# Performance work log

Hardware: AMD Instinct MI355X
Metric: run time of the kernel (lower is better)

## Reference

```python
import jax, jax.numpy as jnp
import numpy as np

H = 64          # HIDDEN_SIZE
D = 300         # WORD_VEC_DIMS
L = 3           # NUM_LSTM_LAYERS
B = 256
T = 512


def _uniform(key, shape, scale):
    return jax.random.uniform(key, shape, jnp.float32, -scale, scale)


def setup_inputs() -> dict:
    key = jax.random.key(0)
    keys = jax.random.split(key, 32)
    s = 1.0 / np.sqrt(H)  # torch LSTM/Linear init scale
    inp = {
        "input": jax.random.normal(keys[0], (B, T, D), jnp.float32),
        "h_0": jnp.zeros((L, B, H), jnp.float32),
        "c_0": jnp.zeros((L, B, H), jnp.float32),
    }
    k = 1
    for l in range(L):
        din = D if l == 0 else H
        inp[f"wih{l}"] = _uniform(keys[k], (4 * H, din), s); k += 1
        inp[f"whh{l}"] = _uniform(keys[k], (4 * H, H), s); k += 1
        inp[f"bih{l}"] = _uniform(keys[k], (4 * H,), s); k += 1
        inp[f"bhh{l}"] = _uniform(keys[k], (4 * H,), s); k += 1
    inp["w1"] = _uniform(keys[k], (H, H), s); k += 1
    inp["b1"] = _uniform(keys[k], (H,), s); k += 1
    inp["w2"] = _uniform(keys[k], (D, H), s); k += 1
    inp["b2"] = _uniform(keys[k], (D,), s); k += 1
    return inp


def _lstm_layer(x_tbd, h0, c0, Wih, Whh, bih, bhh):
    # x_tbd: [T, B, Din]; precompute input projection outside the scan
    xp = jnp.einsum('tbd,gd->tbg', x_tbd, Wih) + bih  # [T, B, 4H]

    def step(carry, xt):
        h, c = carry
        g = xt + h @ Whh.T + bhh
        i, f, gg, o = jnp.split(g, 4, axis=-1)  # torch gate order: i,f,g,o
        c = jax.nn.sigmoid(f) * c + jax.nn.sigmoid(i) * jnp.tanh(gg)
        h = jax.nn.sigmoid(o) * jnp.tanh(c)
        return (h, c), h

    (hT, cT), hs = jax.lax.scan(step, (h0, c0), xp)
    return hs, hT, cT  # hs: [T, B, H]


def reference(input, h_0, c_0, wih0, whh0, bih0, bhh0, wih1, whh1, bih1, bhh1,
              wih2, whh2, bih2, bhh2, w1, b1, w2, b2):
    wih = [wih0, wih1, wih2]
    whh = [whh0, whh1, whh2]
    bih = [bih0, bih1, bih2]
    bhh = [bhh0, bhh1, bhh2]
    x = jnp.transpose(input, (1, 0, 2))  # [T, B, D]
    hs_n, cs_n = [], []
    for l in range(L):
        x, hT, cT = _lstm_layer(x, h_0[l], c_0[l], wih[l], whh[l], bih[l], bhh[l])
        hs_n.append(hT)
        cs_n.append(cT)
    # x is now [T, B, H] == output.permute(1, 0, 2) of the batch_first LSTM.
    # Faithfully replicate the original permute+view reordering:
    flat = x.reshape(-1, H)                       # time-major flatten
    y = jnp.tanh(flat @ w1.T + b1) @ w2.T + b2    # MLP head
    out = y.reshape(input.shape[0], -1, D)        # reinterpreted batch-major
    h_n = jnp.stack(hs_n)
    c_n = jnp.stack(cs_n)
    return out, h_n, c_n
```

## Files before the change

kernel.cpp:

```cpp
#include <hip/hip_runtime.h>
#include <math.h>


#define TT 512
#define BB 256
#define DD 300
#define HH 64
#define MM (TT * BB)
#define XP 256
#define TC 128
#define NC (TT / TC)

__device__ __forceinline__ float bf2f(unsigned short u) {
    return __uint_as_float(((unsigned int)u) << 16);
}
__device__ __forceinline__ unsigned short f2bf(float f) {
    unsigned int x = __float_as_uint(f);
    x += 0x7FFFu + ((x >> 16) & 1u);
    return (unsigned short)(x >> 16);
}
__device__ __forceinline__ float sigm(float x) { return 1.f / (1.f + __expf(-x)); }
__device__ __forceinline__ float tanh_f(float x) { return 1.f - 2.f / (__expf(2.f * x) + 1.f); }

__device__ __forceinline__ float ld1(const void* p, long long i, int md) {
    return md ? ((const float*)p)[i] : bf2f(((const unsigned short*)p)[i]);
}
__device__ __forceinline__ void ld4v(float* d, const void* p, long long i, int md) {
    if (md) {
        float4 v = *(const float4*)((const float*)p + i);
        d[0] = v.x; d[1] = v.y; d[2] = v.z; d[3] = v.w;
    } else {
        ushort4 u = *(const ushort4*)((const unsigned short*)p + i);
        d[0] = bf2f(u.x); d[1] = bf2f(u.y); d[2] = bf2f(u.z); d[3] = bf2f(u.w);
    }
}

#define FMA4x4(a, bv)                                        \
    acc[0][0] = fmaf((a).x, (bv).x, acc[0][0]);              \
    acc[0][1] = fmaf((a).x, (bv).y, acc[0][1]);              \
    acc[0][2] = fmaf((a).x, (bv).z, acc[0][2]);              \
    acc[0][3] = fmaf((a).x, (bv).w, acc[0][3]);              \
    acc[1][0] = fmaf((a).y, (bv).x, acc[1][0]);              \
    acc[1][1] = fmaf((a).y, (bv).y, acc[1][1]);              \
    acc[1][2] = fmaf((a).y, (bv).z, acc[1][2]);              \
    acc[1][3] = fmaf((a).y, (bv).w, acc[1][3]);              \
    acc[2][0] = fmaf((a).z, (bv).x, acc[2][0]);              \
    acc[2][1] = fmaf((a).z, (bv).y, acc[2][1]);              \
    acc[2][2] = fmaf((a).z, (bv).z, acc[2][2]);              \
    acc[2][3] = fmaf((a).z, (bv).w, acc[2][3]);              \
    acc[3][0] = fmaf((a).w, (bv).x, acc[3][0]);              \
    acc[3][1] = fmaf((a).w, (bv).y, acc[3][1]);              \
    acc[3][2] = fmaf((a).w, (bv).z, acc[3][2]);              \
    acc[3][3] = fmaf((a).w, (bv).w, acc[3][3]);

__global__ void detect_kernel(const void* inp, int* mode) {
    if (threadIdx.x == 0 && blockIdx.x == 0) {
        const unsigned short* u = (const unsigned short*)inp;
        int bad = 0;
        for (int i = 0; i < 256; ++i) {
            float f = bf2f(u[i]);
            if (!(f == f) || fabsf(f) > 1e6f) ++bad;
        }
        *mode = (bad >= 4) ? 1 : 0;
    }
}

__global__ __launch_bounds__(256) void init_state(
    const void* h0, const void* c0, float* hstate, float* cstate, const int* modep)
{
    const int md = *modep;
    int i = blockIdx.x * 256 + threadIdx.x;
    if (i < 3 * BB * HH) {
        hstate[i] = ld1(h0, i, md);
        cstate[i] = ld1(c0, i, md);
    }
}

__global__ __launch_bounds__(256) void final_state(
    const float* hstate, const float* cstate, void* out, const int* modep)
{
    const int md = *modep;
    int i = blockIdx.x * 256 + threadIdx.x;
    const long long base = (long long)MM * DD;
    if (i < 3 * BB * HH) {
        if (md) {
            ((float*)out)[base + i] = hstate[i];
            ((float*)out)[base + 3 * BB * HH + i] = cstate[i];
        } else {
            ((unsigned short*)out)[base + i] = f2bf(hstate[i]);
            ((unsigned short*)out)[base + 3 * BB * HH + i] = f2bf(cstate[i]);
        }
    }
}

__global__ __launch_bounds__(256) void proj0_chunk(
    const void* __restrict__ inp, const void* __restrict__ wih,
    const void* __restrict__ bih, const void* __restrict__ bhh,
    float* __restrict__ xp, const int* modep, int chunk)
{
    const int md = *modep;
    __shared__ __align__(16) float At[64][68];
    __shared__ __align__(16) float Wt[64][68];
    const int tid = threadIdx.x;
    const int lr = tid >> 2;
    const int lc = (tid & 3) * 16;
    const int tx = tid & 15, ty = tid >> 4;
    const int m0 = blockIdx.x * 64, n0 = blockIdx.y * 64;
    const int ml = m0 + lr;
    const int b = ml & 255;
    const int t = chunk * TC + (ml >> 8);
    const long long abase = (long long)b * (TT * DD) + (long long)t * DD;
    const long long wbase = (long long)(n0 + lr) * DD;
    float acc[4][4] = {{0.f,0.f,0.f,0.f},{0.f,0.f,0.f,0.f},{0.f,0.f,0.f,0.f},{0.f,0.f,0.f,0.f}};
    for (int k0 = 0; k0 < DD; k0 += 64) {
        if (k0 + lc + 15 < DD) {
            #pragma unroll
            for (int q = 0; q < 4; ++q) {
                float va[4], vw[4];
                ld4v(va, inp, abase + k0 + lc + q * 4, md);
                ld4v(vw, wih, wbase + k0 + lc + q * 4, md);
                #pragma unroll
                for (int e = 0; e < 4; ++e) {
                    At[lc + q * 4 + e][lr] = va[e];
                    Wt[lc + q * 4 + e][lr] = vw[e];
                }
            }
        } else {
            #pragma unroll
            for (int q = 0; q < 16; ++q) {
                int k = k0 + lc + q;
                At[lc + q][lr] = (k < DD) ? ld1(inp, abase + k, md) : 0.f;
                Wt[lc + q][lr] = (k < DD) ? ld1(wih, wbase + k, md) : 0.f;
            }
        }
        __syncthreads();
        #pragma unroll 16
        for (int k = 0; k < 64; ++k) {
            float4 a = *(const float4*)&At[k][ty * 4];
            float4 bv = *(const float4*)&Wt[k][tx * 4];
            FMA4x4(a, bv)
        }
        __syncthreads();
    }
    float bias[4];
    #pragma unroll
    for (int j = 0; j < 4; ++j) {
        int n = n0 + tx * 4 + j;
        bias[j] = ld1(bih, n, md) + ld1(bhh, n, md);
    }
    #pragma unroll
    for (int i = 0; i < 4; ++i) {
        long long row = m0 + ty * 4 + i;
        float4 o = make_float4(acc[i][0] + bias[0], acc[i][1] + bias[1],
                               acc[i][2] + bias[2], acc[i][3] + bias[3]);
        *(float4*)(xp + row * XP + n0 + tx * 4) = o;
    }
}

__global__ __launch_bounds__(256) void projh_chunk(
    const float* __restrict__ A, const void* __restrict__ wih,
    const void* __restrict__ bih, const void* __restrict__ bhh,
    float* __restrict__ xp, const int* modep)
{
    const int md = *modep;
    __shared__ __align__(16) float At[64][68];
    __shared__ __align__(16) float Wt[64][68];
    const int tid = threadIdx.x;
    const int lr = tid >> 2;
    const int lc = (tid & 3) * 16;
    const int tx = tid & 15, ty = tid >> 4;
    const int m0 = blockIdx.x * 64, n0 = blockIdx.y * 64;
    float acc[4][4] = {{0.f,0.f,0.f,0.f},{0.f,0.f,0.f,0.f},{0.f,0.f,0.f,0.f},{0.f,0.f,0.f,0.f}};
    #pragma unroll
    for (int q = 0; q < 4; ++q) {
        float4 av = *(const float4*)(A + (long long)(m0 + lr) * HH + lc + q * 4);
        float vw[4];
        ld4v(vw, wih, (long long)(n0 + lr) * HH + lc + q * 4, md);
        At[lc+q*4+0][lr]=av.x; At[lc+q*4+1][lr]=av.y; At[lc+q*4+2][lr]=av.z; At[lc+q*4+3][lr]=av.w;
        Wt[lc+q*4+0][lr]=vw[0]; Wt[lc+q*4+1][lr]=vw[1]; Wt[lc+q*4+2][lr]=vw[2]; Wt[lc+q*4+3][lr]=vw[3];
    }
    __syncthreads();
    #pragma unroll 16
    for (int k = 0; k < 64; ++k) {
        float4 a = *(const float4*)&At[k][ty * 4];
        float4 bv = *(const float4*)&Wt[k][tx * 4];
        FMA4x4(a, bv)
    }
    float bias[4];
    #pragma unroll
    for (int j = 0; j < 4; ++j) {
        int n = n0 + tx * 4 + j;
        bias[j] = ld1(bih, n, md) + ld1(bhh, n, md);
    }
    #pragma unroll
    for (int i = 0; i < 4; ++i) {
        long long row = m0 + ty * 4 + i;
        float4 o = make_float4(acc[i][0] + bias[0], acc[i][1] + bias[1],
                               acc[i][2] + bias[2], acc[i][3] + bias[3]);
        *(float4*)(xp + row * XP + n0 + tx * 4) = o;
    }
}

__global__ __launch_bounds__(256) void scan_chunk(
    const float* __restrict__ xp, float* __restrict__ hs,
    const void* __restrict__ whh,
    float* __restrict__ hstate, float* __restrict__ cstate, const int* modep)
{
    const int md = *modep;
    const int b = blockIdx.x;
    const int j = threadIdx.x;
    const int g = ((j & 3) << 6) | (j >> 2);
    const int m = j & 63;
    __shared__ __align__(16) float h_s[64];
    __shared__ __align__(16) float g_s[2][256];
    float w[64];
    #pragma unroll
    for (int q = 0; q < 16; ++q) {
        float v[4];
        ld4v(v, whh, (long long)g * HH + q * 4, md);
        w[4*q+0]=v[0]; w[4*q+1]=v[1]; w[4*q+2]=v[2]; w[4*q+3]=v[3];
    }
    float c = cstate[b * HH + m];
    h_s[m] = hstate[b * HH + m];
    float hval = h_s[m];

    const int type = j & 3;
    const float aa = (type == 2) ? 2.f : 1.f;
    const float cc = 1.f - aa;

    const long long xbase = (long long)b * XP + g;
    const long long xstep = (long long)BB * XP;
    float xc[8], xn[8];
    #pragma unroll
    for (int p = 0; p < 8; ++p) xc[p] = xp[xbase + (long long)p * xstep];

    for (int tg = 0; tg < TC; tg += 8) {
        if (tg + 8 < TC) {
            #pragma unroll
            for (int p = 0; p < 8; ++p)
                xn[p] = xp[xbase + (long long)(tg + 8 + p) * xstep];
        }
        #pragma unroll
        for (int u = 0; u < 8; ++u) {
            const int t = tg + u;
            float a0 = xc[u], a1 = 0.f, a2 = 0.f, a3 = 0.f;
            const float4* h4 = (const float4*)h_s;
            #pragma unroll
            for (int q = 0; q < 16; ++q) {
                float4 hv = h4[q];
                a0 = fmaf(hv.x, w[4*q+0], a0);
                a1 = fmaf(hv.y, w[4*q+1], a1);
                a2 = fmaf(hv.z, w[4*q+2], a2);
                a3 = fmaf(hv.w, w[4*q+3], a3);
            }
            float gr = (a0 + a1) + (a2 + a3);
            float s = 1.f / (1.f + __expf(-aa * gr));
            g_s[t & 1][j] = fmaf(aa, s, cc);
            asm volatile("s_waitcnt lgkmcnt(0)\n\ts_barrier" ::: "memory");
            float4 gv = *(const float4*)&g_s[t & 1][4 * m];
            c = gv.y * c + gv.x * gv.z;
            hval = gv.w * tanh_f(c);
            h_s[m] = hval;
            if (j < 64) hs[((long long)t * BB + b) * HH + m] = hval;
        }
        #pragma unroll
        for (int p = 0; p < 8; ++p) xc[p] = xn[p];
    }
    if (j < 64) {
        hstate[b * HH + m] = hval;
        cstate[b * HH + m] = c;
    }
}

__global__ __launch_bounds__(256) void head_chunk(
    const float* __restrict__ hs, const void* __restrict__ w1,
    const void* __restrict__ b1, const void* __restrict__ w2,
    const void* __restrict__ b2, void* __restrict__ out,
    const int* modep, int chunk)
{
    const int md = *modep;
    __shared__ __align__(16) float Ht[64][68];
    __shared__ __align__(16) float Wt[64][68];
    __shared__ __align__(16) float Zt[64][68];
    const int tid = threadIdx.x;
    const int lr = tid >> 2;
    const int lc = (tid & 3) * 16;
    const int tx = tid & 15, ty = tid >> 4;
    const int m0 = blockIdx.x * 64;
    const long long gbase = (long long)chunk * TC * BB;
    #pragma unroll
    for (int q = 0; q < 4; ++q) {
        float4 av = *(const float4*)(hs + (long long)(m0 + lr) * HH + lc + q * 4);
        float vw[4];
        ld4v(vw, w1, (long long)lr * HH + lc + q * 4, md);
        Ht[lc+q*4+0][lr]=av.x; Ht[lc+q*4+1][lr]=av.y; Ht[lc+q*4+2][lr]=av.z; Ht[lc+q*4+3][lr]=av.w;
        Wt[lc+q*4+0][lr]=vw[0]; Wt[lc+q*4+1][lr]=vw[1]; Wt[lc+q*4+2][lr]=vw[2]; Wt[lc+q*4+3][lr]=vw[3];
    }
    __syncthreads();
    {
        float acc[4][4] = {{0.f,0.f,0.f,0.f},{0.f,0.f,0.f,0.f},{0.f,0.f,0.f,0.f},{0.f,0.f,0.f,0.f}};
        #pragma unroll 16
        for (int k = 0; k < 64; ++k) {
            float4 a = *(const float4*)&Ht[k][ty * 4];
            float4 bv = *(const float4*)&Wt[k][tx * 4];
            FMA4x4(a, bv)
        }
        #pragma unroll
        for (int jj = 0; jj < 4; ++jj) {
            float bb = ld1(b1, tx * 4 + jj, md);
            #pragma unroll
            for (int ii = 0; ii < 4; ++ii)
                Zt[tx * 4 + jj][ty * 4 + ii] = tanh_f(acc[ii][jj] + bb);
        }
    }
    __syncthreads();
    for (int dt = 0; dt < 5; ++dt) {
        const int d0 = dt * 64;
        if (d0 + lr < DD) {
            #pragma unroll
            for (int q = 0; q < 4; ++q) {
                float vw[4];
                ld4v(vw, w2, (long long)(d0 + lr) * HH + lc + q * 4, md);
                Wt[lc+q*4+0][lr]=vw[0]; Wt[lc+q*4+1][lr]=vw[1];
                Wt[lc+q*4+2][lr]=vw[2]; Wt[lc+q*4+3][lr]=vw[3];
            }
        }
        __syncthreads();
        float acc[4][4] = {{0.f,0.f,0.f,0.f},{0.f,0.f,0.f,0.f},{0.f,0.f,0.f,0.f},{0.f,0.f,0.f,0.f}};
        #pragma unroll 16
        for (int k = 0; k < 64; ++k) {
            float4 a = *(const float4*)&Zt[k][ty * 4];
            float4 bv = *(const float4*)&Wt[k][tx * 4];
            FMA4x4(a, bv)
        }
        const int d = d0 + tx * 4;
        if (d < DD) {
            float bb0 = ld1(b2, d + 0, md), bb1 = ld1(b2, d + 1, md);
            float bb2v = ld1(b2, d + 2, md), bb3 = ld1(b2, d + 3, md);
            #pragma unroll
            for (int ii = 0; ii < 4; ++ii) {
                long long row = gbase + m0 + ty * 4 + ii;
                float o0 = acc[ii][0] + bb0, o1 = acc[ii][1] + bb1;
                float o2 = acc[ii][2] + bb2v, o3 = acc[ii][3] + bb3;
                if (md) {
                    *(float4*)((float*)out + row * DD + d) = make_float4(o0, o1, o2, o3);
                } else {
                    ushort4 o;
                    o.x = f2bf(o0); o.y = f2bf(o1); o.z = f2bf(o2); o.w = f2bf(o3);
                    *(ushort4*)((unsigned short*)out + row * DD + d) = o;
                }
            }
        }
        __syncthreads();
    }
}

extern "C" void kernel_launch(void* const* d_in, const int* in_sizes, int n_in,
                              void* d_out, int out_size, void* d_ws, size_t ws_size,
                              hipStream_t stream)
{
    const void* inp  = d_in[0];
    const void* h0   = d_in[1];
    const void* c0   = d_in[2];
    const void* wih0 = d_in[3];
    const void* whh0 = d_in[4];
    const void* bih0 = d_in[5];
    const void* bhh0 = d_in[6];
    const void* wih1 = d_in[7];
    const void* whh1 = d_in[8];
    const void* bih1 = d_in[9];
    const void* bhh1 = d_in[10];
    const void* wih2 = d_in[11];
    const void* whh2 = d_in[12];
    const void* bih2 = d_in[13];
    const void* bhh2 = d_in[14];
    const void* w1   = d_in[15];
    const void* b1   = d_in[16];
    const void* w2   = d_in[17];
    const void* b2   = d_in[18];

    int* mode = (int*)d_ws;
    float* wsf = (float*)d_ws;
    float* hstate = wsf + 16;
    float* cstate = hstate + 3 * BB * HH;
    float* xp  = cstate + 3 * BB * HH;
    float* hs0 = xp + (size_t)TC * BB * XP;
    float* hs1 = hs0 + (size_t)TC * BB * HH;
    float* hs2 = hs1 + (size_t)TC * BB * HH;

    detect_kernel<<<1, 64, 0, stream>>>(inp, mode);
    init_state<<<192, 256, 0, stream>>>(h0, c0, hstate, cstate, mode);

    for (int c = 0; c < NC; ++c) {
        proj0_chunk<<<dim3(TC * BB / 64, 4), 256, 0, stream>>>(
            inp, wih0, bih0, bhh0, xp, mode, c);
        scan_chunk<<<BB, 256, 0, stream>>>(
            xp, hs0, whh0, hstate, cstate, mode);
        projh_chunk<<<dim3(TC * BB / 64, 4), 256, 0, stream>>>(
            hs0, wih1, bih1, bhh1, xp, mode);
        scan_chunk<<<BB, 256, 0, stream>>>(
            xp, hs1, whh1, hstate + BB * HH, cstate + BB * HH, mode);
        projh_chunk<<<dim3(TC * BB / 64, 4), 256, 0, stream>>>(
            hs1, wih2, bih2, bhh2, xp, mode);
        scan_chunk<<<BB, 256, 0, stream>>>(
            xp, hs2, whh2, hstate + 2 * BB * HH, cstate + 2 * BB * HH, mode);
        head_chunk<<<TC * BB / 64, 256, 0, stream>>>(
            hs2, w1, b1, w2, b2, d_out, mode, c);
    }
    final_state<<<192, 256, 0, stream>>>(hstate, cstate, d_out, mode);
}
```

Measured before the change: 1.974 ms.

## Use bf16 MFMA for input projections and MLP head in bf16 mode

```diff
diff --git a/kernel.cpp b/kernel.cpp
--- a/kernel.cpp
+++ b/kernel.cpp
@@ -11,6 +11,9 @@
 #define TC 128
 #define NC (TT / TC)
 
+typedef __attribute__((ext_vector_type(8))) short bf16x8;
+typedef __attribute__((ext_vector_type(4))) float f32x4;
+
 __device__ __forceinline__ float bf2f(unsigned short u) {
     return __uint_as_float(((unsigned int)u) << 16);
 }
@@ -33,6 +36,10 @@
         ushort4 u = *(const ushort4*)((const unsigned short*)p + i);
         d[0] = bf2f(u.x); d[1] = bf2f(u.y); d[2] = bf2f(u.z); d[3] = bf2f(u.w);
     }
+}
+
+__device__ __forceinline__ f32x4 mfma16(bf16x8 a, bf16x8 b, f32x4 c) {
+    return __builtin_amdgcn_mfma_f32_16x16x32_bf16(a, b, c, 0, 0, 0);
 }
 
 #define FMA4x4(a, bv)                                        \
@@ -99,61 +106,134 @@
     float* __restrict__ xp, const int* modep, int chunk)
 {
     const int md = *modep;
-    __shared__ __align__(16) float At[64][68];
-    __shared__ __align__(16) float Wt[64][68];
+    __shared__ __align__(16) char smem[46080];
     const int tid = threadIdx.x;
-    const int lr = tid >> 2;
-    const int lc = (tid & 3) * 16;
-    const int tx = tid & 15, ty = tid >> 4;
-    const int m0 = blockIdx.x * 64, n0 = blockIdx.y * 64;
-    const int ml = m0 + lr;
-    const int b = ml & 255;
-    const int t = chunk * TC + (ml >> 8);
-    const long long abase = (long long)b * (TT * DD) + (long long)t * DD;
-    const long long wbase = (long long)(n0 + lr) * DD;
-    float acc[4][4] = {{0.f,0.f,0.f,0.f},{0.f,0.f,0.f,0.f},{0.f,0.f,0.f,0.f},{0.f,0.f,0.f,0.f}};
-    for (int k0 = 0; k0 < DD; k0 += 64) {
-        if (k0 + lc + 15 < DD) {
+    const int m0 = blockIdx.x * 64;
+    if (md == 0) {
+        unsigned short* As = (unsigned short*)smem;
+        unsigned short* Ws = (unsigned short*)smem + 64 * 72;
+        const int lane = tid & 63;
+        const int wv = tid >> 6;
+        const int fr = lane & 15, fq = lane >> 4;
+        const int ar = tid >> 2;
+        const int aq = (tid & 3) << 4;
+        const int ml = m0 + ar;
+        const int b = ml & 255;
+        const int t = chunk * TC + (ml >> 8);
+        const unsigned short* gA = (const unsigned short*)inp +
+            (long long)b * (TT * DD) + (long long)t * DD;
+        const unsigned short* gW = (const unsigned short*)wih + (long long)tid * DD;
+        float bias[4];
+        #pragma unroll
+        for (int nf = 0; nf < 4; ++nf) {
+            int n = wv * 64 + nf * 16 + fr;
+            bias[nf] = ld1(bih, n, 0) + ld1(bhh, n, 0);
+        }
+        f32x4 acc[4][4] = {};
+        for (int k0 = 0; k0 < 320; k0 += 64) {
             #pragma unroll
             for (int q = 0; q < 4; ++q) {
-                float va[4], vw[4];
-                ld4v(va, inp, abase + k0 + lc + q * 4, md);
-                ld4v(vw, wih, wbase + k0 + lc + q * 4, md);
-                #pragma unroll
-                for (int e = 0; e < 4; ++e) {
-                    At[lc + q * 4 + e][lr] = va[e];
-                    Wt[lc + q * 4 + e][lr] = vw[e];
-                }
-            }
-        } else {
+                int kg = k0 + aq + q * 4;
+                ushort4 v = (kg < DD) ? *(const ushort4*)(gA + kg)
+                                      : make_ushort4(0, 0, 0, 0);
+                *(ushort4*)(As + ar * 72 + aq + q * 4) = v;
+            }
             #pragma unroll
             for (int q = 0; q < 16; ++q) {
-                int k = k0 + lc + q;
-                At[lc + q][lr] = (k < DD) ? ld1(inp, abase + k, md) : 0.f;
-                Wt[lc + q][lr] = (k < DD) ? ld1(wih, wbase + k, md) : 0.f;
-            }
-        }
-        __syncthreads();
-        #pragma unroll 16
-        for (int k = 0; k < 64; ++k) {
-            float4 a = *(const float4*)&At[k][ty * 4];
-            float4 bv = *(const float4*)&Wt[k][tx * 4];
-            FMA4x4(a, bv)
-        }
-        __syncthreads();
-    }
-    float bias[4];
-    #pragma unroll
-    for (int j = 0; j < 4; ++j) {
-        int n = n0 + tx * 4 + j;
-        bias[j] = ld1(bih, n, md) + ld1(bhh, n, md);
-    }
-    #pragma unroll
-    for (int i = 0; i < 4; ++i) {
-        long long row = m0 + ty * 4 + i;
-        float4 o = make_float4(acc[i][0] + bias[0], acc[i][1] + bias[1],
-                               acc[i][2] + bias[2], acc[i][3] + bias[3]);
-        *(float4*)(xp + row * XP + n0 + tx * 4) = o;
+                int kg = k0 + q * 4;
+                ushort4 v = (kg < DD) ? *(const ushort4*)(gW + kg)
+                                      : make_ushort4(0, 0, 0, 0);
+                *(ushort4*)(Ws + tid * 72 + q * 4) = v;
+            }
+            __syncthreads();
+            #pragma unroll
+            for (int kf = 0; kf < 2; ++kf) {
+                bf16x8 bfr[4], afr[4];
+                #pragma unroll
+                for (int nf = 0; nf < 4; ++nf)
+                    bfr[nf] = *(const bf16x8*)(Ws + (wv * 64 + nf * 16 + fr) * 72 + kf * 32 + fq * 8);
+                #pragma unroll
+                for (int mf = 0; mf < 4; ++mf)
+                    afr[mf] = *(const bf16x8*)(As + (mf * 16 + fr) * 72 + kf * 32 + fq * 8);
+                #pragma unroll
+                for (int mf = 0; mf < 4; ++mf) {
+                    #pragma unroll
+                    for (int nf = 0; nf < 4; ++nf)
+                        acc[mf][nf] = mfma16(afr[mf], bfr[nf], acc[mf][nf]);
+                }
+            }
+            __syncthreads();
+        }
+        #pragma unroll
+        for (int mf = 0; mf < 4; ++mf) {
+            #pragma unroll
+            for (int nf = 0; nf < 4; ++nf) {
+                const int col = wv * 64 + nf * 16 + fr;
+                #pragma unroll
+                for (int r = 0; r < 4; ++r) {
+                    const int row = m0 + mf * 16 + fq * 4 + r;
+                    xp[(long long)row * XP + col] = acc[mf][nf][r] + bias[nf];
+                }
+            }
+        }
+    } else {
+        float (*At)[68] = (float (*)[68])smem;
+        float (*Wt)[68] = (float (*)[68])(smem + 64 * 68 * 4);
+        const int lr = tid >> 2;
+        const int lc = (tid & 3) * 16;
+        const int tx = tid & 15, ty = tid >> 4;
+        const int ml = m0 + lr;
+        const int b = ml & 255;
+        const int t = chunk * TC + (ml >> 8);
+        const long long abase = (long long)b * (TT * DD) + (long long)t * DD;
+        for (int ny = 0; ny < 4; ++ny) {
+            const int n0 = ny * 64;
+            const long long wbase = (long long)(n0 + lr) * DD;
+            float acc[4][4] = {{0.f,0.f,0.f,0.f},{0.f,0.f,0.f,0.f},{0.f,0.f,0.f,0.f},{0.f,0.f,0.f,0.f}};
+            for (int k0 = 0; k0 < DD; k0 += 64) {
+                if (k0 + lc + 15 < DD) {
+                    #pragma unroll
+                    for (int q = 0; q < 4; ++q) {
+                        float va[4], vw[4];
+                        ld4v(va, inp, abase + k0 + lc + q * 4, md);
+                        ld4v(vw, wih, wbase + k0 + lc + q * 4, md);
+                        #pragma unroll
+                        for (int e = 0; e < 4; ++e) {
+                            At[lc + q * 4 + e][lr] = va[e];
+                            Wt[lc + q * 4 + e][lr] = vw[e];
+                        }
+                    }
+                } else {
+                    #pragma unroll
+                    for (int q = 0; q < 16; ++q) {
+                        int k = k0 + lc + q;
+                        At[lc + q][lr] = (k < DD) ? ld1(inp, abase + k, md) : 0.f;
+                        Wt[lc + q][lr] = (k < DD) ? ld1(wih, wbase + k, md) : 0.f;
+                    }
+                }
+                __syncthreads();
+                #pragma unroll 16
+                for (int k = 0; k < 64; ++k) {
+                    float4 a = *(const float4*)&At[k][ty * 4];
+                    float4 bv = *(const float4*)&Wt[k][tx * 4];
+                    FMA4x4(a, bv)
+                }
+                __syncthreads();
+            }
+            float bias[4];
+            #pragma unroll
+            for (int j = 0; j < 4; ++j) {
+                int n = n0 + tx * 4 + j;
+                bias[j] = ld1(bih, n, md) + ld1(bhh, n, md);
+            }
+            #pragma unroll
+            for (int i = 0; i < 4; ++i) {
+                long long row = m0 + ty * 4 + i;
+                float4 o = make_float4(acc[i][0] + bias[0], acc[i][1] + bias[1],
+                                       acc[i][2] + bias[2], acc[i][3] + bias[3]);
+                *(float4*)(xp + row * XP + n0 + tx * 4) = o;
+            }
+        }
     }
 }
 
@@ -163,41 +243,116 @@
     float* __restrict__ xp, const int* modep)
 {
     const int md = *modep;
-    __shared__ __align__(16) float At[64][68];
-    __shared__ __align__(16) float Wt[64][68];
+    __shared__ __align__(16) char smem[55296];
     const int tid = threadIdx.x;
-    const int lr = tid >> 2;
-    const int lc = (tid & 3) * 16;
-    const int tx = tid & 15, ty = tid >> 4;
-    const int m0 = blockIdx.x * 64, n0 = blockIdx.y * 64;
-    float acc[4][4] = {{0.f,0.f,0.f,0.f},{0.f,0.f,0.f,0.f},{0.f,0.f,0.f,0.f},{0.f,0.f,0.f,0.f}};
-    #pragma unroll
-    for (int q = 0; q < 4; ++q) {
-        float4 av = *(const float4*)(A + (long long)(m0 + lr) * HH + lc + q * 4);
-        float vw[4];
-        ld4v(vw, wih, (long long)(n0 + lr) * HH + lc + q * 4, md);
-        At[lc+q*4+0][lr]=av.x; At[lc+q*4+1][lr]=av.y; At[lc+q*4+2][lr]=av.z; At[lc+q*4+3][lr]=av.w;
-        Wt[lc+q*4+0][lr]=vw[0]; Wt[lc+q*4+1][lr]=vw[1]; Wt[lc+q*4+2][lr]=vw[2]; Wt[lc+q*4+3][lr]=vw[3];
-    }
-    __syncthreads();
-    #pragma unroll 16
-    for (int k = 0; k < 64; ++k) {
-        float4 a = *(const float4*)&At[k][ty * 4];
-        float4 bv = *(const float4*)&Wt[k][tx * 4];
-        FMA4x4(a, bv)
-    }
-    float bias[4];
-    #pragma unroll
-    for (int j = 0; j < 4; ++j) {
-        int n = n0 + tx * 4 + j;
-        bias[j] = ld1(bih, n, md) + ld1(bhh, n, md);
-    }
-    #pragma unroll
-    for (int i = 0; i < 4; ++i) {
-        long long row = m0 + ty * 4 + i;
-        float4 o = make_float4(acc[i][0] + bias[0], acc[i][1] + bias[1],
-                               acc[i][2] + bias[2], acc[i][3] + bias[3]);
-        *(float4*)(xp + row * XP + n0 + tx * 4) = o;
+    const int m0 = blockIdx.x * 64;
+    if (md == 0) {
+        unsigned short* Ahi = (unsigned short*)smem;
+        unsigned short* Alo = Ahi + 64 * 72;
+        unsigned short* Ws  = Alo + 64 * 72;
+        const int lane = tid & 63, wv = tid >> 6;
+        const int fr = lane & 15, fq = lane >> 4;
+        const int ar = tid >> 2, aq = (tid & 3) << 4;
+        #pragma unroll
+        for (int q = 0; q < 4; ++q) {
+            float4 v = *(const float4*)(A + (long long)(m0 + ar) * HH + aq + q * 4);
+            ushort4 hi, lo;
+            hi.x = f2bf(v.x); lo.x = f2bf(v.x - bf2f(hi.x));
+            hi.y = f2bf(v.y); lo.y = f2bf(v.y - bf2f(hi.y));
+            hi.z = f2bf(v.z); lo.z = f2bf(v.z - bf2f(hi.z));
+            hi.w = f2bf(v.w); lo.w = f2bf(v.w - bf2f(hi.w));
+            *(ushort4*)(Ahi + ar * 72 + aq + q * 4) = hi;
+            *(ushort4*)(Alo + ar * 72 + aq + q * 4) = lo;
+        }
+        {
+            const uint4* gw = (const uint4*)((const unsigned short*)wih + (long long)tid * HH);
+            #pragma unroll
+            for (int q = 0; q < 8; ++q)
+                *(uint4*)(Ws + tid * 72 + q * 8) = gw[q];
+        }
+        float bias[4];
+        #pragma unroll
+        for (int nf = 0; nf < 4; ++nf) {
+            int n = wv * 64 + nf * 16 + fr;
+            bias[nf] = ld1(bih, n, 0) + ld1(bhh, n, 0);
+        }
+        __syncthreads();
+        bf16x8 bfr[4][2];
+        #pragma unroll
+        for (int nf = 0; nf < 4; ++nf) {
+            #pragma unroll
+            for (int kf = 0; kf < 2; ++kf)
+                bfr[nf][kf] = *(const bf16x8*)(Ws + (wv * 64 + nf * 16 + fr) * 72 + kf * 32 + fq * 8);
+        }
+        f32x4 acc[4][4] = {};
+        #pragma unroll
+        for (int mf = 0; mf < 4; ++mf) {
+            bf16x8 ah[2], al[2];
+            #pragma unroll
+            for (int kf = 0; kf < 2; ++kf) {
+                ah[kf] = *(const bf16x8*)(Ahi + (mf * 16 + fr) * 72 + kf * 32 + fq * 8);
+                al[kf] = *(const bf16x8*)(Alo + (mf * 16 + fr) * 72 + kf * 32 + fq * 8);
+            }
+            #pragma unroll
+            for (int nf = 0; nf < 4; ++nf) {
+                #pragma unroll
+                for (int kf = 0; kf < 2; ++kf) {
+                    acc[mf][nf] = mfma16(ah[kf], bfr[nf][kf], acc[mf][nf]);
+                    acc[mf][nf] = mfma16(al[kf], bfr[nf][kf], acc[mf][nf]);
+                }
+            }
+        }
+        #pragma unroll
+        for (int mf = 0; mf < 4; ++mf) {
+            #pragma unroll
+            for (int nf = 0; nf < 4; ++nf) {
+                const int col = wv * 64 + nf * 16 + fr;
+                #pragma unroll
+                for (int r = 0; r < 4; ++r) {
+                    const int row = m0 + mf * 16 + fq * 4 + r;
+                    xp[(long long)row * XP + col] = acc[mf][nf][r] + bias[nf];
+                }
+            }
+        }
+    } else {
+        float (*At)[68] = (float (*)[68])smem;
+        float (*Wt)[68] = (float (*)[68])(smem + 64 * 68 * 4);
+        const int lr = tid >> 2;
+        const int lc = (tid & 3) * 16;
+        const int tx = tid & 15, ty = tid >> 4;
+        for (int ny = 0; ny < 4; ++ny) {
+            const int n0 = ny * 64;
+            #pragma unroll
+            for (int q = 0; q < 4; ++q) {
+                float4 av = *(const float4*)(A + (long long)(m0 + lr) * HH + lc + q * 4);
+                float vw[4];
+                ld4v(vw, wih, (long long)(n0 + lr) * HH + lc + q * 4, md);
+                At[lc+q*4+0][lr]=av.x; At[lc+q*4+1][lr]=av.y; At[lc+q*4+2][lr]=av.z; At[lc+q*4+3][lr]=av.w;
+                Wt[lc+q*4+0][lr]=vw[0]; Wt[lc+q*4+1][lr]=vw[1]; Wt[lc+q*4+2][lr]=vw[2]; Wt[lc+q*4+3][lr]=vw[3];
+            }
+            __syncthreads();
+            float acc[4][4] = {{0.f,0.f,0.f,0.f},{0.f,0.f,0.f,0.f},{0.f,0.f,0.f,0.f},{0.f,0.f,0.f,0.f}};
+            #pragma unroll 16
+            for (int k = 0; k < 64; ++k) {
+                float4 a = *(const float4*)&At[k][ty * 4];
+                float4 bv = *(const float4*)&Wt[k][tx * 4];
+                FMA4x4(a, bv)
+            }
+            float bias[4];
+            #pragma unroll
+            for (int j = 0; j < 4; ++j) {
+                int n = n0 + tx * 4 + j;
+                bias[j] = ld1(bih, n, md) + ld1(bhh, n, md);
+            }
+            #pragma unroll
+            for (int i = 0; i < 4; ++i) {
+                long long row = m0 + ty * 4 + i;
+                float4 o = make_float4(acc[i][0] + bias[0], acc[i][1] + bias[1],
+                                       acc[i][2] + bias[2], acc[i][3] + bias[3]);
+                *(float4*)(xp + row * XP + n0 + tx * 4) = o;
+            }
+            __syncthreads();
+        }
     }
 }
 
@@ -279,79 +434,181 @@
     const int* modep, int chunk)
 {
     const int md = *modep;
-    __shared__ __align__(16) float Ht[64][68];
-    __shared__ __align__(16) float Wt[64][68];
-    __shared__ __align__(16) float Zt[64][68];
+    __shared__ __align__(16) char smem[52224];
     const int tid = threadIdx.x;
-    const int lr = tid >> 2;
-    const int lc = (tid & 3) * 16;
-    const int tx = tid & 15, ty = tid >> 4;
     const int m0 = blockIdx.x * 64;
     const long long gbase = (long long)chunk * TC * BB;
-    #pragma unroll
-    for (int q = 0; q < 4; ++q) {
-        float4 av = *(const float4*)(hs + (long long)(m0 + lr) * HH + lc + q * 4);
-        float vw[4];
-        ld4v(vw, w1, (long long)lr * HH + lc + q * 4, md);
-        Ht[lc+q*4+0][lr]=av.x; Ht[lc+q*4+1][lr]=av.y; Ht[lc+q*4+2][lr]=av.z; Ht[lc+q*4+3][lr]=av.w;
-        Wt[lc+q*4+0][lr]=vw[0]; Wt[lc+q*4+1][lr]=vw[1]; Wt[lc+q*4+2][lr]=vw[2]; Wt[lc+q*4+3][lr]=vw[3];
-    }
-    __syncthreads();
-    {
-        float acc[4][4] = {{0.f,0.f,0.f,0.f},{0.f,0.f,0.f,0.f},{0.f,0.f,0.f,0.f},{0.f,0.f,0.f,0.f}};
-        #pragma unroll 16
-        for (int k = 0; k < 64; ++k) {
-            float4 a = *(const float4*)&Ht[k][ty * 4];
-            float4 bv = *(const float4*)&Wt[k][tx * 4];
-            FMA4x4(a, bv)
-        }
-        #pragma unroll
-        for (int jj = 0; jj < 4; ++jj) {
-            float bb = ld1(b1, tx * 4 + jj, md);
-            #pragma unroll
-            for (int ii = 0; ii < 4; ++ii)
-                Zt[tx * 4 + jj][ty * 4 + ii] = tanh_f(acc[ii][jj] + bb);
-        }
-    }
-    __syncthreads();
-    for (int dt = 0; dt < 5; ++dt) {
-        const int d0 = dt * 64;
-        if (d0 + lr < DD) {
-            #pragma unroll
-            for (int q = 0; q < 4; ++q) {
-                float vw[4];
-                ld4v(vw, w2, (long long)(d0 + lr) * HH + lc + q * 4, md);
-                Wt[lc+q*4+0][lr]=vw[0]; Wt[lc+q*4+1][lr]=vw[1];
-                Wt[lc+q*4+2][lr]=vw[2]; Wt[lc+q*4+3][lr]=vw[3];
-            }
+    if (md == 0) {
+        unsigned short* Ahi = (unsigned short*)smem;
+        unsigned short* Alo = Ahi + 4608;
+        unsigned short* Ws  = Alo + 4608;
+        unsigned short* Zhi = Ws + 4608;
+        unsigned short* Zlo = Zhi + 4608;
+        const int lane = tid & 63, wv = tid >> 6;
+        const int fr = lane & 15, fq = lane >> 4;
+        const int ar = tid >> 2, aq = (tid & 3) << 4;
+        #pragma unroll
+        for (int q = 0; q < 4; ++q) {
+            float4 v = *(const float4*)(hs + (long long)(m0 + ar) * HH + aq + q * 4);
+            ushort4 hi, lo;
+            hi.x = f2bf(v.x); lo.x = f2bf(v.x - bf2f(hi.x));
+            hi.y = f2bf(v.y); lo.y = f2bf(v.y - bf2f(hi.y));
+            hi.z = f2bf(v.z); lo.z = f2bf(v.z - bf2f(hi.z));
+            hi.w = f2bf(v.w); lo.w = f2bf(v.w - bf2f(hi.w));
+            *(ushort4*)(Ahi + ar * 72 + aq + q * 4) = hi;
+            *(ushort4*)(Alo + ar * 72 + aq + q * 4) = lo;
+        }
+        {
+            const uint4* g1 = (const uint4*)((const unsigned short*)w1 + ar * HH + aq);
+            *(uint4*)(Ws + ar * 72 + aq) = g1[0];
+            *(uint4*)(Ws + ar * 72 + aq + 8) = g1[1];
         }
         __syncthreads();
-        float acc[4][4] = {{0.f,0.f,0.f,0.f},{0.f,0.f,0.f,0.f},{0.f,0.f,0.f,0.f},{0.f,0.f,0.f,0.f}};
-        #pragma unroll 16
-        for (int k = 0; k < 64; ++k) {
-            float4 a = *(const float4*)&Zt[k][ty * 4];
-            float4 bv = *(const float4*)&Wt[k][tx * 4];
-            FMA4x4(a, bv)
-        }
-        const int d = d0 + tx * 4;
-        if (d < DD) {
-            float bb0 = ld1(b2, d + 0, md), bb1 = ld1(b2, d + 1, md);
-            float bb2v = ld1(b2, d + 2, md), bb3 = ld1(b2, d + 3, md);
-            #pragma unroll
-            for (int ii = 0; ii < 4; ++ii) {
-                long long row = gbase + m0 + ty * 4 + ii;
-                float o0 = acc[ii][0] + bb0, o1 = acc[ii][1] + bb1;
-                float o2 = acc[ii][2] + bb2v, o3 = acc[ii][3] + bb3;
-                if (md) {
-                    *(float4*)((float*)out + row * DD + d) = make_float4(o0, o1, o2, o3);
-                } else {
-                    ushort4 o;
-                    o.x = f2bf(o0); o.y = f2bf(o1); o.z = f2bf(o2); o.w = f2bf(o3);
-                    *(ushort4*)((unsigned short*)out + row * DD + d) = o;
+        {
+            f32x4 acc[4] = {};
+            bf16x8 ah[2], al[2];
+            #pragma unroll
+            for (int kf = 0; kf < 2; ++kf) {
+                ah[kf] = *(const bf16x8*)(Ahi + (wv * 16 + fr) * 72 + kf * 32 + fq * 8);
+                al[kf] = *(const bf16x8*)(Alo + (wv * 16 + fr) * 72 + kf * 32 + fq * 8);
+            }
+            #pragma unroll
+            for (int nf = 0; nf < 4; ++nf) {
+                #pragma unroll
+                for (int kf = 0; kf < 2; ++kf) {
+                    bf16x8 bfr = *(const bf16x8*)(Ws + (nf * 16 + fr) * 72 + kf * 32 + fq * 8);
+                    acc[nf] = mfma16(ah[kf], bfr, acc[nf]);
+                    acc[nf] = mfma16(al[kf], bfr, acc[nf]);
+                }
+            }
+            #pragma unroll
+            for (int nf = 0; nf < 4; ++nf) {
+                float bb = ld1(b1, nf * 16 + fr, 0);
+                #pragma unroll
+                for (int r = 0; r < 4; ++r) {
+                    float z = tanh_f(acc[nf][r] + bb);
+                    unsigned short h = f2bf(z);
+                    int zi = (wv * 16 + fq * 4 + r) * 72 + nf * 16 + fr;
+                    Zhi[zi] = h;
+                    Zlo[zi] = f2bf(z - bf2f(h));
                 }
             }
         }
         __syncthreads();
+        bf16x8 zh[2], zl[2];
+        #pragma unroll
+        for (int kf = 0; kf < 2; ++kf) {
+            zh[kf] = *(const bf16x8*)(Zhi + (wv * 16 + fr) * 72 + kf * 32 + fq * 8);
+            zl[kf] = *(const bf16x8*)(Zlo + (wv * 16 + fr) * 72 + kf * 32 + fq * 8);
+        }
+        for (int dt = 0; dt < 5; ++dt) {
+            const int n = dt * 64 + ar;
+            if (n < DD) {
+                const uint4* g2 = (const uint4*)((const unsigned short*)w2 + (long long)n * HH + aq);
+                *(uint4*)(Ws + ar * 72 + aq) = g2[0];
+                *(uint4*)(Ws + ar * 72 + aq + 8) = g2[1];
+            } else {
+                uint4 zv = make_uint4(0, 0, 0, 0);
+                *(uint4*)(Ws + ar * 72 + aq) = zv;
+                *(uint4*)(Ws + ar * 72 + aq + 8) = zv;
+            }
+            __syncthreads();
+            f32x4 acc[4] = {};
+            #pragma unroll
+            for (int nf = 0; nf < 4; ++nf) {
+                #pragma unroll
+                for (int kf = 0; kf < 2; ++kf) {
+                    bf16x8 bfr = *(const bf16x8*)(Ws + (nf * 16 + fr) * 72 + kf * 32 + fq * 8);
+                    acc[nf] = mfma16(zh[kf], bfr, acc[nf]);
+                    acc[nf] = mfma16(zl[kf], bfr, acc[nf]);
+                }
+            }
+            #pragma unroll
+            for (int nf = 0; nf < 4; ++nf) {
+                const int col = dt * 64 + nf * 16 + fr;
+                if (col < DD) {
+                    float bb = ld1(b2, col, 0);
+                    #pragma unroll
+                    for (int r = 0; r < 4; ++r) {
+                        long long row = gbase + m0 + wv * 16 + fq * 4 + r;
+                        ((unsigned short*)out)[row * DD + col] = f2bf(acc[nf][r] + bb);
+                    }
+                }
+            }
+            __syncthreads();
+        }
+    } else {
+        float (*Ht)[68] = (float (*)[68])smem;
+        float (*Wt)[68] = (float (*)[68])(smem + 17408);
+        float (*Zt)[68] = (float (*)[68])(smem + 34816);
+        const int lr = tid >> 2;
+        const int lc = (tid & 3) * 16;
+        const int tx = tid & 15, ty = tid >> 4;
+        #pragma unroll
+        for (int q = 0; q < 4; ++q) {
+            float4 av = *(const float4*)(hs + (long long)(m0 + lr) * HH + lc + q * 4);
+            float vw[4];
+            ld4v(vw, w1, (long long)lr * HH + lc + q * 4, md);
+            Ht[lc+q*4+0][lr]=av.x; Ht[lc+q*4+1][lr]=av.y; Ht[lc+q*4+2][lr]=av.z; Ht[lc+q*4+3][lr]=av.w;
+            Wt[lc+q*4+0][lr]=vw[0]; Wt[lc+q*4+1][lr]=vw[1]; Wt[lc+q*4+2][lr]=vw[2]; Wt[lc+q*4+3][lr]=vw[3];
+        }
+        __syncthreads();
+        {
+            float acc[4][4] = {{0.f,0.f,0.f,0.f},{0.f,0.f,0.f,0.f},{0.f,0.f,0.f,0.f},{0.f,0.f,0.f,0.f}};
+            #pragma unroll 16
+            for (int k = 0; k < 64; ++k) {
+                float4 a = *(const float4*)&Ht[k][ty * 4];
+                float4 bv = *(const float4*)&Wt[k][tx * 4];
+                FMA4x4(a, bv)
+            }
+            #pragma unroll
+            for (int jj = 0; jj < 4; ++jj) {
+                float bb = ld1(b1, tx * 4 + jj, md);
+                #pragma unroll
+                for (int ii = 0; ii < 4; ++ii)
+                    Zt[tx * 4 + jj][ty * 4 + ii] = tanh_f(acc[ii][jj] + bb);
+            }
+        }
+        __syncthreads();
+        for (int dt = 0; dt < 5; ++dt) {
+            const int d0 = dt * 64;
+            if (d0 + lr < DD) {
+                #pragma unroll
+                for (int q = 0; q < 4; ++q) {
+                    float vw[4];
+                    ld4v(vw, w2, (long long)(d0 + lr) * HH + lc + q * 4, md);
+                    Wt[lc+q*4+0][lr]=vw[0]; Wt[lc+q*4+1][lr]=vw[1];
+                    Wt[lc+q*4+2][lr]=vw[2]; Wt[lc+q*4+3][lr]=vw[3];
+                }
+            }
+            __syncthreads();
+            float acc[4][4] = {{0.f,0.f,0.f,0.f},{0.f,0.f,0.f,0.f},{0.f,0.f,0.f,0.f},{0.f,0.f,0.f,0.f}};
+            #pragma unroll 16
+            for (int k = 0; k < 64; ++k) {
+                float4 a = *(const float4*)&Zt[k][ty * 4];
+                float4 bv = *(const float4*)&Wt[k][tx * 4];
+                FMA4x4(a, bv)
+            }
+            const int d = d0 + tx * 4;
+            if (d < DD) {
+                float bb0 = ld1(b2, d + 0, md), bb1 = ld1(b2, d + 1, md);
+                float bb2v = ld1(b2, d + 2, md), bb3 = ld1(b2, d + 3, md);
+                #pragma unroll
+                for (int ii = 0; ii < 4; ++ii) {
+                    long long row = gbase + m0 + ty * 4 + ii;
+                    float o0 = acc[ii][0] + bb0, o1 = acc[ii][1] + bb1;
+                    float o2 = acc[ii][2] + bb2v, o3 = acc[ii][3] + bb3;
+                    if (md) {
+                        *(float4*)((float*)out + row * DD + d) = make_float4(o0, o1, o2, o3);
+                    } else {
+                        ushort4 o;
+                        o.x = f2bf(o0); o.y = f2bf(o1); o.z = f2bf(o2); o.w = f2bf(o3);
+                        *(ushort4*)((unsigned short*)out + row * DD + d) = o;
+                    }
+                }
+            }
+            __syncthreads();
+        }
     }
 }
 
@@ -392,15 +649,15 @@
     init_state<<<192, 256, 0, stream>>>(h0, c0, hstate, cstate, mode);
 
     for (int c = 0; c < NC; ++c) {
-        proj0_chunk<<<dim3(TC * BB / 64, 4), 256, 0, stream>>>(
+        proj0_chunk<<<dim3(TC * BB / 64), 256, 0, stream>>>(
             inp, wih0, bih0, bhh0, xp, mode, c);
         scan_chunk<<<BB, 256, 0, stream>>>(
             xp, hs0, whh0, hstate, cstate, mode);
-        projh_chunk<<<dim3(TC * BB / 64, 4), 256, 0, stream>>>(
+        projh_chunk<<<dim3(TC * BB / 64), 256, 0, stream>>>(
             hs0, wih1, bih1, bhh1, xp, mode);
         scan_chunk<<<BB, 256, 0, stream>>>(
             xp, hs1, whh1, hstate + BB * HH, cstate + BB * HH, mode);
-        projh_chunk<<<dim3(TC * BB / 64, 4), 256, 0, stream>>>(
+        projh_chunk<<<dim3(TC * BB / 64), 256, 0, stream>>>(
             hs1, wih2, bih2, bhh2, xp, mode);
         scan_chunk<<<BB, 256, 0, stream>>>(
             xp, hs2, whh2, hstate + 2 * BB * HH, cstate + 2 * BB * HH, mode);
```

Measured after the change: 2.010 ms. No clear change (+1.8%).
